# Kernel optimization log

Measured on AMD Instinct MI355X. Metric: run time of the kernel, lower is better.

The kernel has to match this reference:

```python
import jax, jax.numpy as jnp
import numpy as np
import math

B = 2        # batch
S = 4095     # input sequence (cls token makes L = 4096)
F_IN = 32    # input feature size
D = 512      # d_model (hidden_size)
H = 8        # n_heads
E = D // H   # head dim = 64
DFF = 2048   # feedforward dim
NL = 2       # encoder layers
FACTOR = 5   # probsparse sampling factor
EPS = 1e-5


def setup_inputs() -> dict:
    key = jax.random.key(0)
    ks = jax.random.split(key, 16)

    def w(k, shape):
        return jax.random.normal(k, shape, dtype=jnp.float32) * 0.02

    inp = {}
    inp['x'] = jax.random.normal(ks[0], (B, S, F_IN), dtype=jnp.float32)
    inp['We'] = w(ks[1], (D, F_IN)); inp['be'] = jnp.zeros((D,), jnp.float32)
    inp['cls'] = jnp.zeros((1, 1, D), jnp.float32)
    inp['Wq'] = w(ks[2], (NL, D, D)); inp['bq'] = jnp.zeros((NL, D), jnp.float32)
    inp['Wk'] = w(ks[3], (NL, D, D)); inp['bk'] = jnp.zeros((NL, D), jnp.float32)
    inp['Wv'] = w(ks[4], (NL, D, D)); inp['bv'] = jnp.zeros((NL, D), jnp.float32)
    inp['Wo'] = w(ks[5], (NL, D, D)); inp['bo'] = jnp.zeros((NL, D), jnp.float32)
    inp['g1'] = jnp.ones((NL, D), jnp.float32); inp['b1'] = jnp.zeros((NL, D), jnp.float32)
    inp['g2'] = jnp.ones((NL, D), jnp.float32); inp['b2'] = jnp.zeros((NL, D), jnp.float32)
    inp['W1'] = w(ks[6], (NL, DFF, D)); inp['bf1'] = jnp.zeros((NL, DFF), jnp.float32)
    inp['W2'] = w(ks[7], (NL, D, DFF)); inp['bf2'] = jnp.zeros((NL, D), jnp.float32)
    inp['Wf'] = w(ks[8], (1, D)); inp['bf'] = jnp.zeros((1,), jnp.float32)
    return inp


def pos_encoding(L):
    # Sinusoidal positional encoding [L, D]
    pos = jnp.arange(L, dtype=jnp.float32)[:, None]
    div = jnp.exp(jnp.arange(0, D, 2, dtype=jnp.float32) * (-math.log(10000.0) / D))
    pe = jnp.zeros((L, D), jnp.float32)
    pe = pe.at[:, 0::2].set(jnp.sin(pos * div))
    pe = pe.at[:, 1::2].set(jnp.cos(pos * div))
    return pe


def layer_norm(x, g, b):
    mu = x.mean(-1, keepdims=True)
    var = ((x - mu) ** 2).mean(-1, keepdims=True)
    return (x - mu) / jnp.sqrt(var + EPS) * g + b


def prob_attention(q, k, v, rng):
    # q, k, v: [B, H, L, E]; mask_flag=False (encoder self-attention)
    b, h, L, e = q.shape
    u = min(FACTOR * int(np.ceil(np.log(L))), L)  # sample_k == n_top here (L_Q == L_K)
    idx = jax.random.randint(rng, (L, u), 0, L)   # random K sampling per query position
    Ks = k[:, :, idx, :]                          # [B,H,L,u,E] gather
    QKs = jnp.einsum('bhle,bhlue->bhlu', q, Ks)   # sampled scores
    M = QKs.max(-1) - QKs.sum(-1) / L             # sparsity measure [B,H,L]
    _, top = jax.lax.top_k(M, u)                  # active query indices [B,H,u]
    Qr = jnp.take_along_axis(q, top[..., None], axis=2)      # [B,H,u,E]
    scores = jnp.einsum('bhue,bhke->bhuk', Qr, k) / math.sqrt(e)
    attn = jax.nn.softmax(scores, axis=-1)
    ctx = jnp.broadcast_to(v.mean(axis=2, keepdims=True), (b, h, L, e))  # initial context = mean(V)
    upd = jnp.einsum('bhuk,bhke->bhue', attn, v)
    bi = jnp.arange(b)[:, None, None]
    hi = jnp.arange(h)[None, :, None]
    ctx = ctx.at[bi, hi, top].set(upd)            # scatter active-query contexts
    return ctx                                    # [B,H,L,E]


def attention_layer(x, Wq_, bq_, Wk_, bk_, Wv_, bv_, Wo_, bo_, rng):
    b, L, _ = x.shape
    q = (x @ Wq_.T + bq_).reshape(b, L, H, E).transpose(0, 2, 1, 3)
    k = (x @ Wk_.T + bk_).reshape(b, L, H, E).transpose(0, 2, 1, 3)
    v = (x @ Wv_.T + bv_).reshape(b, L, H, E).transpose(0, 2, 1, 3)
    ctx = prob_attention(q, k, v, rng)            # [B,H,L,E]
    out = ctx.transpose(0, 2, 1, 3).reshape(b, L, D)
    return out @ Wo_.T + bo_


def reference(x, We, be, cls, Wq, bq, Wk, bk, Wv, bv, Wo, bo, g1, b1, g2, b2, W1, bf1, W2, bf2, Wf, bf):
    h = x @ We.T + be                                            # [B,S,D]
    h = jnp.concatenate([jnp.broadcast_to(cls, (B, 1, D)), h], axis=1)  # prepend cls
    L = h.shape[1]
    h = h + pos_encoding(L)[None]
    for l in range(NL):
        rng = jax.random.fold_in(jax.random.key(42), l)
        a = attention_layer(h, Wq[l], bq[l], Wk[l], bk[l], Wv[l], bv[l], Wo[l], bo[l], rng)
        h = layer_norm(h + a, g1[l], b1[l])
        y = jax.nn.relu(h @ W1[l].T + bf1[l])
        y = y @ W2[l].T + bf2[l]
        h = layer_norm(h + y, g2[l], b2[l])
    return h[:, 0] @ Wf.T + bf  # cls-token prediction head [B,1]
```

## Files before the change

### kernel.cpp

```cpp
#include <hip/hip_runtime.h>
#include <hip/hip_bf16.h>
#include <math.h>
#include <stdint.h>

#define B 2
#define S 4095
#define LSEQ 4096
#define F_IN 32
#define D 512
#define H 8
#define E 64
#define DFF 2048
#define NL 2
#define U 45
#define EPSL 1e-5f
#define LU (LSEQ * U)
#define HALF_LU (LU / 2)
#define NS 32
#define SLICE 128
#define CASTBLK 3074

typedef __attribute__((ext_vector_type(8))) short short8;
typedef __attribute__((ext_vector_type(4))) float f32x4;

#define GLD(gp, lp)                                                            \
    __builtin_amdgcn_global_load_lds(                                          \
        (const __attribute__((address_space(1))) void*)(gp),                   \
        (__attribute__((address_space(3))) void*)(lp), 16, 0, 0)

__device__ __forceinline__ unsigned short bf16_bits(float f) {
    __hip_bfloat16 h = __float2bfloat16(f);
    return *(unsigned short*)&h;
}
__device__ __forceinline__ float bits_to_f32(unsigned short s) {
    union { uint32_t u; float f; } c;
    c.u = ((uint32_t)s) << 16;
    return c.f;
}
__device__ __forceinline__ unsigned long long mkey(float v, int index) {
    uint32_t u = __float_as_uint(v);
    uint32_t mono = (u & 0x80000000u) ? ~u : (u | 0x80000000u);
    return ((unsigned long long)mono << 32) | (uint32_t)(0xFFFFFFFFu - (uint32_t)index);
}

#define TF_BODY(k0, k1, c0, c1, o0, o1)                                        \
    do {                                                                       \
        uint32_t ks2 = (k0) ^ (k1) ^ 0x1BD11BDAu;                              \
        uint32_t x0 = (c0) + (k0), x1 = (c1) + (k1);                           \
        x0 += x1; x1 = ((x1 << 13) | (x1 >> 19)); x1 ^= x0;                    \
        x0 += x1; x1 = ((x1 << 15) | (x1 >> 17)); x1 ^= x0;                    \
        x0 += x1; x1 = ((x1 << 26) | (x1 >> 6));  x1 ^= x0;                    \
        x0 += x1; x1 = ((x1 << 6) | (x1 >> 26));  x1 ^= x0;                    \
        x0 += (k1); x1 += ks2 + 1u;                                            \
        x0 += x1; x1 = ((x1 << 17) | (x1 >> 15)); x1 ^= x0;                    \
        x0 += x1; x1 = ((x1 << 29) | (x1 >> 3));  x1 ^= x0;                    \
        x0 += x1; x1 = ((x1 << 16) | (x1 >> 16)); x1 ^= x0;                    \
        x0 += x1; x1 = ((x1 << 24) | (x1 >> 8));  x1 ^= x0;                    \
        x0 += ks2; x1 += (k0) + 2u;                                            \
        x0 += x1; x1 = ((x1 << 13) | (x1 >> 19)); x1 ^= x0;                    \
        x0 += x1; x1 = ((x1 << 15) | (x1 >> 17)); x1 ^= x0;                    \
        x0 += x1; x1 = ((x1 << 26) | (x1 >> 6));  x1 ^= x0;                    \
        x0 += x1; x1 = ((x1 << 6) | (x1 >> 26));  x1 ^= x0;                    \
        x0 += (k0); x1 += (k1) + 3u;                                           \
        x0 += x1; x1 = ((x1 << 17) | (x1 >> 15)); x1 ^= x0;                    \
        x0 += x1; x1 = ((x1 << 29) | (x1 >> 3));  x1 ^= x0;                    \
        x0 += x1; x1 = ((x1 << 16) | (x1 >> 16)); x1 ^= x0;                    \
        x0 += x1; x1 = ((x1 << 24) | (x1 >> 8));  x1 ^= x0;                    \
        x0 += (k1); x1 += ks2 + 4u;                                            \
        x0 += x1; x1 = ((x1 << 13) | (x1 >> 19)); x1 ^= x0;                    \
        x0 += x1; x1 = ((x1 << 15) | (x1 >> 17)); x1 ^= x0;                    \
        x0 += x1; x1 = ((x1 << 26) | (x1 >> 6));  x1 ^= x0;                    \
        x0 += x1; x1 = ((x1 << 6) | (x1 >> 26));  x1 ^= x0;                    \
        x0 += ks2; x1 += (k0) + 5u;                                            \
        (o0) = x0; (o1) = x1;                                                  \
    } while (0)

__device__ __forceinline__ void threefry_dev(uint32_t k0, uint32_t k1, uint32_t c0,
                                             uint32_t c1, uint32_t& o0, uint32_t& o1) {
    TF_BODY(k0, k1, c0, c1, o0, o1);
}
static void threefry_host(uint32_t k0, uint32_t k1, uint32_t c0, uint32_t c1,
                          uint32_t& o0, uint32_t& o1) {
    TF_BODY(k0, k1, c0, c1, o0, o1);
}

__global__ void prep_cast_kernel(const float* __restrict__ x, const float* __restrict__ We,
                                 __hip_bfloat16* __restrict__ xbf,
                                 __hip_bfloat16* __restrict__ webf,
                                 const float* __restrict__ Wq,
                                 const float* __restrict__ Wk,
                                 const float* __restrict__ Wv,
                                 const float* __restrict__ Wo,
                                 const float* __restrict__ W1,
                                 const float* __restrict__ W2,
                                 const float* __restrict__ bq,
                                 const float* __restrict__ bk,
                                 const float* __restrict__ bv,
                                 __hip_bfloat16* __restrict__ wpool,
                                 float* __restrict__ qkvbias) {
    const int SDD = D * D / 4;
    const int SFD = DFF * D / 4;
    const int CAST_N = 4 * SDD + 2 * SFD;
    const size_t WPL = (size_t)4 * D * D + 2 * (size_t)DFF * D;
    int bid = blockIdx.x;
    int tid = threadIdx.x;
    if (bid < 2 * CASTBLK) {
        int l = bid / CASTBLK;
        int u = (bid % CASTBLK) * 256 + tid;
        __hip_bfloat16* base = wpool + (size_t)l * WPL;
        if (u >= CAST_N) {
            int j = u - CAST_N;
            if (j < 384) {
                int seg = (j * 4) >> 9;
                int off = (j * 4) & 511;
                const float* src = (seg == 0) ? bq + l * D
                                 : (seg == 1) ? bk + l * D : bv + l * D;
                *(float4*)(qkvbias + l * 1536 + j * 4) = *(const float4*)(src + off);
            }
            return;
        }
        const float* src;
        __hip_bfloat16* dst;
        int off;
        if (u < SDD)            { src = Wq + (size_t)l * D * D;   dst = base;                       off = u; }
        else if (u < 2 * SDD)   { src = Wk + (size_t)l * D * D;   dst = base + (size_t)D * D;       off = u - SDD; }
        else if (u < 3 * SDD)   { src = Wv + (size_t)l * D * D;   dst = base + (size_t)2 * D * D;   off = u - 2 * SDD; }
        else if (u < 4 * SDD)   { src = Wo + (size_t)l * D * D;   dst = base + (size_t)3 * D * D;   off = u - 3 * SDD; }
        else if (u < 4 * SDD + SFD) { src = W1 + (size_t)l * DFF * D; dst = base + (size_t)4 * D * D; off = u - 4 * SDD; }
        else { src = W2 + (size_t)l * D * DFF; dst = base + (size_t)4 * D * D + (size_t)DFF * D; off = u - 4 * SDD - SFD; }
        float4 v = ((const float4*)src)[off];
        union { unsigned short s[4]; uint2 w; } o;
        o.s[0] = bf16_bits(v.x); o.s[1] = bf16_bits(v.y);
        o.s[2] = bf16_bits(v.z); o.s[3] = bf16_bits(v.w);
        ((uint2*)dst)[off] = o.w;
    } else {
        int u = (bid - 2 * CASTBLK) * 256 + tid;
        const int NX = B * LSEQ * F_IN / 4;
        const int NW = D * F_IN / 4;
        if (u < NX) {
            int e0 = u * 4;
            int i = e0 & 31;
            int l = (e0 >> 5) & (LSEQ - 1);
            int b = e0 >> 17;
            union { unsigned short s[4]; uint2 w; } o;
            if (l == 0) {
                o.s[0] = o.s[1] = o.s[2] = o.s[3] = 0;
            } else {
                float4 v = *(const float4*)(x + ((size_t)b * S + (l - 1)) * F_IN + i);
                o.s[0] = bf16_bits(v.x); o.s[1] = bf16_bits(v.y);
                o.s[2] = bf16_bits(v.z); o.s[3] = bf16_bits(v.w);
            }
            ((uint2*)xbf)[u] = o.w;
        } else if (u < NX + NW) {
            int w = u - NX;
            float4 v = ((const float4*)We)[w];
            union { unsigned short s[4]; uint2 w2; } o;
            o.s[0] = bf16_bits(v.x); o.s[1] = bf16_bits(v.y);
            o.s[2] = bf16_bits(v.z); o.s[3] = bf16_bits(v.w);
            ((uint2*)webf)[w] = o.w2;
        }
    }
}

__global__ __launch_bounds__(256) void gemm32(const unsigned short* __restrict__ A,
                                              const unsigned short* __restrict__ W,
                                              const float* __restrict__ bias,
                                              float* __restrict__ Cf,
                                              int M, int N, int K) {
    __shared__ unsigned short lds[2 * 128 * 32];
    unsigned short* As = lds;
    unsigned short* Bs = lds + 128 * 32;
    const int tid = threadIdx.x;
    const int m0 = blockIdx.y * 128, n0 = blockIdx.x * 128;
    const int wave = tid >> 6, lane = tid & 63;
    const int wm = (wave >> 1) * 64, wn = (wave & 1) * 64;
    const int quad = lane >> 4, m15 = lane & 15;
    const int srow = tid >> 2, scol = (tid & 3) * 8;
    f32x4 acc[4][4] = {};
    const unsigned short* Ag0 = A + (size_t)(m0 + srow) * K + scol;
    const unsigned short* Ag1 = A + (size_t)(m0 + srow + 64) * K + scol;
    const unsigned short* Wg0 = W + (size_t)(n0 + srow) * K + scol;
    const unsigned short* Wg1 = W + (size_t)(n0 + srow + 64) * K + scol;
    for (int k0 = 0; k0 < K; k0 += 32) {
        __syncthreads();
        GLD(Ag0 + k0, As + tid * 8);
        GLD(Ag1 + k0, As + 2048 + tid * 8);
        GLD(Wg0 + k0, Bs + tid * 8);
        GLD(Wg1 + k0, Bs + 2048 + tid * 8);
        __syncthreads();
        short8 af[4], bfr[4];
#pragma unroll
        for (int mi = 0; mi < 4; ++mi)
            af[mi] = *(const short8*)(As + (wm + mi * 16 + m15) * 32 + quad * 8);
#pragma unroll
        for (int ni = 0; ni < 4; ++ni)
            bfr[ni] = *(const short8*)(Bs + (wn + ni * 16 + m15) * 32 + quad * 8);
#pragma unroll
        for (int mi = 0; mi < 4; ++mi)
#pragma unroll
            for (int ni = 0; ni < 4; ++ni)
                acc[mi][ni] = __builtin_amdgcn_mfma_f32_16x16x32_bf16(
                    af[mi], bfr[ni], acc[mi][ni], 0, 0, 0);
    }
#pragma unroll
    for (int mi = 0; mi < 4; ++mi) {
        int mg = m0 + wm + mi * 16 + quad * 4;
#pragma unroll
        for (int ni = 0; ni < 4; ++ni) {
            int ng = n0 + wn + ni * 16 + m15;
            float bv = bias[ng];
#pragma unroll
            for (int r = 0; r < 4; ++r)
                Cf[(size_t)(mg + r) * N + ng] = acc[mi][ni][r] + bv;
        }
    }
}

__global__ void posenc_kernel(const float* __restrict__ emb, const float* __restrict__ cls,
                              __hip_bfloat16* __restrict__ hbf) {
    int gid = blockIdx.x * blockDim.x + threadIdx.x;
    if (gid >= B * LSEQ * D) return;
    int d = gid % D;
    int l = (gid / D) % LSEQ;
    float v = (l == 0) ? cls[d] : emb[gid];
    int i = d >> 1;
    float divv = expf((float)(2 * i) * (float)(-9.210340371976184 / 512.0));
    float ang = (float)l * divv;
    v += (d & 1) ? cosf(ang) : sinf(ang);
    hbf[gid] = __float2bfloat16(v);
}

template <int MODE>
__global__ __launch_bounds__(256) void gemm_pipe(const unsigned short* __restrict__ A,
                                                 const unsigned short* __restrict__ W,
                                                 const float* __restrict__ bias,
                                                 void* __restrict__ C0,
                                                 void* __restrict__ C1,
                                                 void* __restrict__ C2,
                                                 int M, int N, int K, int NBN) {
    __shared__ unsigned short As[2][128 * 32];
    __shared__ unsigned short Bs[2][128 * 32];
    const int tid = threadIdx.x;
    const int NBM = M >> 7;
    const int bid = blockIdx.x;
    const int xcd = bid & 7, local = bid >> 3;
    const int m_t = xcd * (NBM >> 3) + local / NBN;
    const int n_t = local % NBN;
    const int m0 = m_t * 128, n0 = n_t * 128;
    const int wave = tid >> 6, lane = tid & 63;
    const int wm = (wave >> 1) * 64, wn = (wave & 1) * 64;
    const int quad = lane >> 4, m15 = lane & 15;
    const int srow = tid >> 2, scol = (tid & 3) * 8;
    f32x4 acc[4][4] = {};
    const unsigned short* Ag0 = A + (size_t)(m0 + srow) * K + scol;
    const unsigned short* Ag1 = A + (size_t)(m0 + srow + 64) * K + scol;
    const unsigned short* Wg0 = W + (size_t)(n0 + srow) * K + scol;
    const unsigned short* Wg1 = W + (size_t)(n0 + srow + 64) * K + scol;
    GLD(Ag0, As[0] + tid * 8);
    GLD(Ag1, As[0] + 2048 + tid * 8);
    GLD(Wg0, Bs[0] + tid * 8);
    GLD(Wg1, Bs[0] + 2048 + tid * 8);
    int cur = 0;
    for (int k0 = 0; k0 < K; k0 += 32) {
        __syncthreads();
        int kn = k0 + 32;
        if (kn < K) {
            GLD(Ag0 + kn, As[cur ^ 1] + tid * 8);
            GLD(Ag1 + kn, As[cur ^ 1] + 2048 + tid * 8);
            GLD(Wg0 + kn, Bs[cur ^ 1] + tid * 8);
            GLD(Wg1 + kn, Bs[cur ^ 1] + 2048 + tid * 8);
        }
        short8 af[4], bfr[4];
#pragma unroll
        for (int mi = 0; mi < 4; ++mi)
            af[mi] = *(const short8*)(As[cur] + (wm + mi * 16 + m15) * 32 + quad * 8);
#pragma unroll
        for (int ni = 0; ni < 4; ++ni)
            bfr[ni] = *(const short8*)(Bs[cur] + (wn + ni * 16 + m15) * 32 + quad * 8);
#pragma unroll
        for (int mi = 0; mi < 4; ++mi)
#pragma unroll
            for (int ni = 0; ni < 4; ++ni)
                acc[mi][ni] = __builtin_amdgcn_mfma_f32_16x16x32_bf16(
                    af[mi], bfr[ni], acc[mi][ni], 0, 0, 0);
        cur ^= 1;
    }
#pragma unroll
    for (int mi = 0; mi < 4; ++mi) {
        int mg = m0 + wm + mi * 16 + quad * 4;
#pragma unroll
        for (int ni = 0; ni < 4; ++ni) {
            int ng = n0 + wn + ni * 16 + m15;
            float bv = bias[ng];
#pragma unroll
            for (int r = 0; r < 4; ++r) {
                float v = acc[mi][ni][r] + bv;
                if (MODE == 1) {
                    ((__hip_bfloat16*)C0)[(size_t)(mg + r) * N + ng] = __float2bfloat16(v);
                } else if (MODE == 2) {
                    ((__hip_bfloat16*)C0)[(size_t)(mg + r) * N + ng] =
                        __float2bfloat16(fmaxf(v, 0.f));
                } else {
                    int seg = ng >> 9;
                    int col = ng & 511;
                    __hip_bfloat16* dst = (seg == 0) ? (__hip_bfloat16*)C0
                                        : (seg == 1) ? (__hip_bfloat16*)C1
                                                     : (__hip_bfloat16*)C2;
                    dst[(size_t)(mg + r) * D + col] = __float2bfloat16(v);
                }
            }
        }
    }
}

__global__ __launch_bounds__(256) void gemm_w2b(const unsigned short* __restrict__ A,
                                                const unsigned short* __restrict__ W,
                                                const float* __restrict__ bias,
                                                float* __restrict__ C0,
                                                float* __restrict__ C1) {
    const int K = 2048, N = 512, KH = 1024;
    __shared__ unsigned short As[2][128 * 32];
    __shared__ unsigned short Bs[2][128 * 32];
    const int tid = threadIdx.x;
    const int bid = blockIdx.x;
    const int xcd = bid & 7, local = bid >> 3;
    const int m_t = xcd * 8 + (local >> 3);
    const int n_t = (local >> 1) & 3;
    const int ks = local & 1;
    const int m0 = m_t * 128, n0 = n_t * 128, kb = ks * KH;
    const int wave = tid >> 6, lane = tid & 63;
    const int wm = (wave >> 1) * 64, wn = (wave & 1) * 64;
    const int quad = lane >> 4, m15 = lane & 15;
    const int srow = tid >> 2, scol = (tid & 3) * 8;
    f32x4 acc[4][4] = {};
    const unsigned short* Ag0 = A + (size_t)(m0 + srow) * K + kb + scol;
    const unsigned short* Ag1 = A + (size_t)(m0 + srow + 64) * K + kb + scol;
    const unsigned short* Wg0 = W + (size_t)(n0 + srow) * K + kb + scol;
    const unsigned short* Wg1 = W + (size_t)(n0 + srow + 64) * K + kb + scol;
    GLD(Ag0, As[0] + tid * 8);
    GLD(Ag1, As[0] + 2048 + tid * 8);
    GLD(Wg0, Bs[0] + tid * 8);
    GLD(Wg1, Bs[0] + 2048 + tid * 8);
    int cur = 0;
    for (int k0 = 0; k0 < KH; k0 += 32) {
        __syncthreads();
        int kn = k0 + 32;
        if (kn < KH) {
            GLD(Ag0 + kn, As[cur ^ 1] + tid * 8);
            GLD(Ag1 + kn, As[cur ^ 1] + 2048 + tid * 8);
            GLD(Wg0 + kn, Bs[cur ^ 1] + tid * 8);
            GLD(Wg1 + kn, Bs[cur ^ 1] + 2048 + tid * 8);
        }
        short8 af[4], bfr[4];
#pragma unroll
        for (int mi = 0; mi < 4; ++mi)
            af[mi] = *(const short8*)(As[cur] + (wm + mi * 16 + m15) * 32 + quad * 8);
#pragma unroll
        for (int ni = 0; ni < 4; ++ni)
            bfr[ni] = *(const short8*)(Bs[cur] + (wn + ni * 16 + m15) * 32 + quad * 8);
#pragma unroll
        for (int mi = 0; mi < 4; ++mi)
#pragma unroll
            for (int ni = 0; ni < 4; ++ni)
                acc[mi][ni] = __builtin_amdgcn_mfma_f32_16x16x32_bf16(
                    af[mi], bfr[ni], acc[mi][ni], 0, 0, 0);
        cur ^= 1;
    }
    float* Cf = ks ? C1 : C0;
#pragma unroll
    for (int mi = 0; mi < 4; ++mi) {
        int mg = m0 + wm + mi * 16 + quad * 4;
#pragma unroll
        for (int ni = 0; ni < 4; ++ni) {
            int ng = n0 + wn + ni * 16 + m15;
            float bv = ks ? 0.f : bias[ng];
#pragma unroll
            for (int r = 0; r < 4; ++r)
                Cf[(size_t)(mg + r) * N + ng] = acc[mi][ni][r] + bv;
        }
    }
}

__global__ __launch_bounds__(256) void mscore_kernel(const __hip_bfloat16* __restrict__ qbf,
                                                     const __hip_bfloat16* __restrict__ kbf,
                                                     uint32_t k2a, uint32_t k2b,
                                                     float* __restrict__ Mv,
                                                     float* __restrict__ acorr) {
    __shared__ float Sbuf[U][8];
    __shared__ int sidx[U];
    int bid = blockIdx.x;
    int tid = threadIdx.x;
    if (bid >= B * LSEQ) {
        int vb = bid - B * LSEQ;
        float4 z = {0.f, 0.f, 0.f, 0.f};
        float4* p = (float4*)acorr;
#pragma unroll
        for (int i = 0; i < 32; ++i)
            p[(size_t)i * 32768 + vb * 256 + tid] = z;
        return;
    }
    int b = bid & 1;
    int l = bid >> 1;
    int wave = tid >> 6, lane = tid & 63;
    if (tid < U) {
        int i = l * U + tid;
        uint32_t c0 = (i < HALF_LU) ? (uint32_t)i : (uint32_t)(i - HALF_LU);
        uint32_t o0, o1;
        threefry_dev(k2a, k2b, c0, c0 + HALF_LU, o0, o1);
        sidx[tid] = (int)(((i < HALF_LU) ? o0 : o1) & 4095u);
    }
    const unsigned short* qr =
        (const unsigned short*)qbf + ((size_t)(b * LSEQ) + l) * D + lane * 8;
    union { uint4 u; unsigned short s[8]; } qv;
    qv.u = *(const uint4*)qr;
    float qa[8];
#pragma unroll
    for (int j = 0; j < 8; ++j) qa[j] = bits_to_f32(qv.s[j]);
    __syncthreads();
    const unsigned short* kbase = (const unsigned short*)(kbf + (size_t)(b * LSEQ) * D);
    for (int t = wave; t < U; t += 12) {
        int tb = t + 4, tc = t + 8;
        bool hb = tb < U, hc = tc < U;
        union { uint4 u; unsigned short s[8]; } kva, kvb, kvc;
        kva.u = *(const uint4*)(kbase + (size_t)sidx[t] * D + lane * 8);
        if (hb) kvb.u = *(const uint4*)(kbase + (size_t)sidx[tb] * D + lane * 8);
        if (hc) kvc.u = *(const uint4*)(kbase + (size_t)sidx[tc] * D + lane * 8);
        {
            float p = 0.f;
#pragma unroll
            for (int j = 0; j < 8; ++j) p += qa[j] * bits_to_f32(kva.s[j]);
            p += __shfl_xor(p, 1);
            p += __shfl_xor(p, 2);
            p += __shfl_xor(p, 4);
            if ((lane & 7) == 0) Sbuf[t][lane >> 3] = p;
        }
        if (hb) {
            float p = 0.f;
#pragma unroll
            for (int j = 0; j < 8; ++j) p += qa[j] * bits_to_f32(kvb.s[j]);
            p += __shfl_xor(p, 1);
            p += __shfl_xor(p, 2);
            p += __shfl_xor(p, 4);
            if ((lane & 7) == 0) Sbuf[tb][lane >> 3] = p;
        }
        if (hc) {
            float p = 0.f;
#pragma unroll
            for (int j = 0; j < 8; ++j) p += qa[j] * bits_to_f32(kvc.s[j]);
            p += __shfl_xor(p, 1);
            p += __shfl_xor(p, 2);
            p += __shfl_xor(p, 4);
            if ((lane & 7) == 0) Sbuf[tc][lane >> 3] = p;
        }
    }
    __syncthreads();
    if (tid < 8) {
        float mx = -INFINITY, sm = 0.f;
        for (int t = 0; t < U; ++t) {
            float v = Sbuf[t][tid];
            mx = fmaxf(mx, v);
            sm += v;
        }
        Mv[((size_t)b * H + tid) * LSEQ + l] = mx - sm / (float)LSEQ;
    }
}

__global__ __launch_bounds__(256) void topk_chunk_kernel(const float* __restrict__ Mv,
                                                         unsigned long long* __restrict__ cand) {
    __shared__ unsigned long long sk[256];
    int blk = blockIdx.x;
    int chunk = blk & 15, bh = blk >> 4;
    int tid = threadIdx.x;
    int gi = chunk * 256 + tid;
    sk[tid] = mkey(Mv[(size_t)bh * LSEQ + gi], gi);
    __syncthreads();
    for (int k = 2; k <= 256; k <<= 1) {
        for (int j = k >> 1; j > 0; j >>= 1) {
            int ixj = tid ^ j;
            if (ixj > tid) {
                unsigned long long a = sk[tid], b = sk[ixj];
                bool desc = ((tid & k) == 0);
                if (desc ? (a < b) : (a > b)) { sk[tid] = b; sk[ixj] = a; }
            }
            __syncthreads();
        }
    }
    if (tid < U) cand[((size_t)bh * 16 + chunk) * U + tid] = sk[tid];
}

__global__ __launch_bounds__(256) void topkmerge_vmean_kernel(
        const unsigned long long* __restrict__ cand, int* __restrict__ top,
        const __hip_bfloat16* __restrict__ v, float* __restrict__ part,
        unsigned char* __restrict__ flags) {
    __shared__ unsigned long long sk[1024];
    __shared__ float red[4][64];
    int blk = blockIdx.x;
    int tid = threadIdx.x;
    if (blk < B * H) {
        int bh = blk;
        for (int e = tid; e < 1024; e += 256)
            sk[e] = (e < 16 * U) ? cand[(size_t)bh * 16 * U + e] : 0ull;
        __syncthreads();
        for (int k = 2; k <= 1024; k <<= 1) {
            for (int j = k >> 1; j > 0; j >>= 1) {
                for (int e = tid; e < 1024; e += 256) {
                    int ixj = e ^ j;
                    if (ixj > e) {
                        unsigned long long a = sk[e], b = sk[ixj];
                        bool desc = ((e & k) == 0);
                        if (desc ? (a < b) : (a > b)) { sk[e] = b; sk[ixj] = a; }
                    }
                }
                __syncthreads();
            }
        }
        if (tid < U)
            top[bh * U + tid] = (int)(0xFFFFFFFFu - (uint32_t)(sk[tid] & 0xFFFFFFFFu));
    } else if (blk < B * H + B * H * 8) {
        int vb = blk - B * H;
        int seg = vb & 7, hh = (vb >> 3) & 7, b = vb >> 6;
        int e = tid & 63, rg = tid >> 6;
        const __hip_bfloat16* vp =
            v + ((size_t)(b * LSEQ) + seg * 512) * D + hh * 64 + e;
        float acc = 0.f;
        for (int r = rg; r < 512; r += 4) acc += __bfloat162float(vp[(size_t)r * D]);
        red[rg][e] = acc;
        __syncthreads();
        if (tid < 64)
            part[(size_t)vb * 64 + tid] =
                red[0][tid] + red[1][tid] + red[2][tid] + red[3][tid];
    } else {
        int fb = blk - (B * H + B * H * 8);
        ((int*)flags)[fb * 256 + tid] = 0;
    }
}

__global__ __launch_bounds__(256) void attnred_wobase_kernel(
        const float* __restrict__ Opart, const float* __restrict__ msum,
        const float* __restrict__ vpart, const unsigned short* __restrict__ wob,
        const int* __restrict__ top, float* __restrict__ acorr,
        unsigned char* __restrict__ flags, const float* __restrict__ bo,
        float* __restrict__ base) {
    __shared__ float dlt[E];
    int bid = blockIdx.x;
    int tid = threadIdx.x;
    if (bid < B * H * U) {
        int t = bid % U;
        int bh = bid / U;
        int b = bh >> 3, hh = bh & 7;
        if (tid < 64) {
            int lane = tid;
            float m_s = -INFINITY, ss = 0.f;
            if (lane < NS) {
                size_t base2 = (((size_t)bh * NS + lane) * U + t) * 2;
                m_s = msum[base2];
                ss = msum[base2 + 1];
            }
            float M = m_s;
            for (int off = 32; off; off >>= 1) M = fmaxf(M, __shfl_xor(M, off));
            float e_s = (lane < NS) ? __expf(m_s - M) : 0.f;
            float d = ss * e_s;
            for (int off = 32; off; off >>= 1) d += __shfl_xor(d, off);
            float acc = 0.f;
            for (int s = 0; s < NS; ++s) {
                float w = __shfl(e_s, s);
                acc += w * Opart[(((size_t)bh * NS + s) * U + t) * 64 + lane];
            }
            float vmv = 0.f;
#pragma unroll
            for (int s = 0; s < 8; ++s) vmv += vpart[((size_t)bh * 8 + s) * 64 + lane];
            dlt[lane] = acc / d - vmv / (float)LSEQ;
        }
        __syncthreads();
        int r = top[bh * U + t];
        if (tid == 0) flags[b * LSEQ + r] = 1;
        float* arow = acorr + (size_t)(b * LSEQ + r) * D;
        for (int n = tid; n < D; n += 256) {
            const unsigned short* wr = wob + (size_t)n * D + hh * E;
            float acc = 0.f;
#pragma unroll
            for (int v4 = 0; v4 < 8; ++v4) {
                union { uint4 u; unsigned short s[8]; } w;
                w.u = *(const uint4*)(wr + v4 * 8);
#pragma unroll
                for (int j = 0; j < 8; ++j)
                    acc += dlt[v4 * 8 + j] * bits_to_f32(w.s[j]);
            }
            atomicAdd(arow + n, acc);
        }
    } else {
        int wb = bid - B * H * U;
        int b = wb >> 7;
        int n = (wb & 127) * 4 + (tid >> 6);
        int lane = tid & 63;
        float vmv[8];
#pragma unroll
        for (int j = 0; j < 8; ++j) {
            int idx = lane * 8 + j;
            int hh = idx >> 6, e = idx & 63;
            float acc = 0.f;
#pragma unroll
            for (int s = 0; s < 8; ++s)
                acc += vpart[((size_t)(b * 8 + hh) * 8 + s) * 64 + e];
            vmv[j] = acc / (float)LSEQ;
        }
        union { uint4 u; unsigned short s[8]; } w;
        w.u = *(const uint4*)(wob + (size_t)n * D + lane * 8);
        float p = vmv[0] * bits_to_f32(w.s[0]) + vmv[1] * bits_to_f32(w.s[1]) +
                  vmv[2] * bits_to_f32(w.s[2]) + vmv[3] * bits_to_f32(w.s[3]) +
                  vmv[4] * bits_to_f32(w.s[4]) + vmv[5] * bits_to_f32(w.s[5]) +
                  vmv[6] * bits_to_f32(w.s[6]) + vmv[7] * bits_to_f32(w.s[7]);
        for (int off = 32; off; off >>= 1) p += __shfl_xor(p, off);
        if (lane == 0) base[(size_t)b * D + n] = p + bo[n];
    }
}

__global__ __launch_bounds__(256) void attn_part(const __hip_bfloat16* __restrict__ qbf,
                                                 const __hip_bfloat16* __restrict__ kbf,
                                                 const __hip_bfloat16* __restrict__ vbf,
                                                 const int* __restrict__ top,
                                                 float* __restrict__ Opart,
                                                 float* __restrict__ msum) {
    __shared__ unsigned short Qs[48 * 72];
    __shared__ unsigned short Ks[SLICE * 72];
    __shared__ unsigned short Vs[SLICE * 68];
    __shared__ unsigned short Ps[48 * 136];
    __shared__ float mred[48][4];
    __shared__ float sred[48][4];
    const int slice = blockIdx.x, hh = blockIdx.y, b = blockIdx.z;
    const int bh = b * H + hh;
    const int tid = threadIdx.x;
    const int s0 = slice * SLICE;
    for (int i = tid; i < 48 * 64; i += 256) {
        int t = i >> 6, e = i & 63;
        unsigned short v = 0;
        if (t < U) {
            int r = top[bh * U + t];
            v = ((const unsigned short*)qbf)[((size_t)(b * LSEQ) + r) * D + hh * E + e];
        }
        Qs[t * 72 + e] = v;
    }
    {
        const uint4* src = (const uint4*)(kbf + ((size_t)(b * LSEQ) + s0) * D + hh * E);
        for (int i = tid; i < SLICE * 8; i += 256) {
            int r = i >> 3, c = i & 7;
            uint4 d = src[(size_t)r * 64 + c];
            *(uint4*)(Ks + r * 72 + c * 8) = d;
        }
    }
    {
        const uint2* src = (const uint2*)(vbf + ((size_t)(b * LSEQ) + s0) * D + hh * E);
        for (int i = tid; i < SLICE * 16; i += 256) {
            int r = i >> 4, c = i & 15;
            uint2 d = src[(size_t)r * 128 + c];
            *(uint2*)(Vs + r * 68 + c * 4) = d;
        }
    }
    __syncthreads();
    const int wave = tid >> 6, lane = tid & 63;
    const int quad = lane >> 4, m15 = lane & 15;
    const int wc = wave * 32;
    f32x4 acc[3][2] = {};
#pragma unroll
    for (int ks = 0; ks < 2; ++ks) {
        short8 af[3], bfr[2];
#pragma unroll
        for (int mt = 0; mt < 3; ++mt)
            af[mt] = *(const short8*)(Qs + (mt * 16 + m15) * 72 + ks * 32 + quad * 8);
#pragma unroll
        for (int nt = 0; nt < 2; ++nt)
            bfr[nt] = *(const short8*)(Ks + (wc + nt * 16 + m15) * 72 + ks * 32 + quad * 8);
#pragma unroll
        for (int mt = 0; mt < 3; ++mt)
#pragma unroll
            for (int nt = 0; nt < 2; ++nt)
                acc[mt][nt] = __builtin_amdgcn_mfma_f32_16x16x32_bf16(
                    af[mt], bfr[nt], acc[mt][nt], 0, 0, 0);
    }
    float sc[3][2][4];
#pragma unroll
    for (int mt = 0; mt < 3; ++mt)
#pragma unroll
        for (int nt = 0; nt < 2; ++nt)
#pragma unroll
            for (int r = 0; r < 4; ++r) sc[mt][nt][r] = acc[mt][nt][r] * 0.125f;
#pragma unroll
    for (int mt = 0; mt < 3; ++mt)
#pragma unroll
        for (int r = 0; r < 4; ++r) {
            float mv = fmaxf(sc[mt][0][r], sc[mt][1][r]);
            mv = fmaxf(mv, __shfl_xor(mv, 1));
            mv = fmaxf(mv, __shfl_xor(mv, 2));
            mv = fmaxf(mv, __shfl_xor(mv, 4));
            mv = fmaxf(mv, __shfl_xor(mv, 8));
            if (m15 == 0) mred[mt * 16 + quad * 4 + r][wave] = mv;
        }
    __syncthreads();
#pragma unroll
    for (int mt = 0; mt < 3; ++mt)
#pragma unroll
        for (int r = 0; r < 4; ++r) {
            int row = mt * 16 + quad * 4 + r;
            float ms = fmaxf(fmaxf(mred[row][0], mred[row][1]),
                             fmaxf(mred[row][2], mred[row][3]));
            float p0 = __expf(sc[mt][0][r] - ms);
            float p1 = __expf(sc[mt][1][r] - ms);
            float sv = p0 + p1;
            sv += __shfl_xor(sv, 1);
            sv += __shfl_xor(sv, 2);
            sv += __shfl_xor(sv, 4);
            sv += __shfl_xor(sv, 8);
            if (m15 == 0) sred[row][wave] = sv;
            Ps[row * 136 + wc + m15] = bf16_bits(p0);
            Ps[row * 136 + wc + 16 + m15] = bf16_bits(p1);
        }
    __syncthreads();
    if (tid < U) {
        float mm = fmaxf(fmaxf(mred[tid][0], mred[tid][1]),
                         fmaxf(mred[tid][2], mred[tid][3]));
        float ss = sred[tid][0] + sred[tid][1] + sred[tid][2] + sred[tid][3];
        size_t base = (((size_t)bh * NS + slice) * U + tid) * 2;
        msum[base] = mm;
        msum[base + 1] = ss;
    }
    f32x4 apv[3] = {};
#pragma unroll
    for (int ks = 0; ks < 4; ++ks) {
        short8 bv;
#pragma unroll
        for (int j = 0; j < 8; ++j)
            bv[j] = (short)Vs[(ks * 32 + quad * 8 + j) * 68 + wave * 16 + m15];
        short8 af2[3];
#pragma unroll
        for (int mt = 0; mt < 3; ++mt)
            af2[mt] = *(const short8*)(Ps + (mt * 16 + m15) * 136 + ks * 32 + quad * 8);
#pragma unroll
        for (int mt = 0; mt < 3; ++mt)
            apv[mt] = __builtin_amdgcn_mfma_f32_16x16x32_bf16(af2[mt], bv, apv[mt], 0, 0, 0);
    }
    size_t obase = ((size_t)bh * NS + slice) * U;
#pragma unroll
    for (int mt = 0; mt < 3; ++mt)
#pragma unroll
        for (int r = 0; r < 4; ++r) {
            int row = mt * 16 + quad * 4 + r;
            if (row < U)
                Opart[(obase + row) * 64 + wave * 16 + m15] = apv[mt][r];
        }
}

__global__ __launch_bounds__(64) void add_ln_base_kernel(__hip_bfloat16* __restrict__ hbf,
                                                         const float* __restrict__ base,
                                                         const float* __restrict__ acorr,
                                                         const unsigned char* __restrict__ flags,
                                                         const float* __restrict__ g,
                                                         const float* __restrict__ bb) {
    int row = blockIdx.x;
    int b = row >> 12;
    int lane = threadIdx.x;
    unsigned short* hp = (unsigned short*)hbf + (size_t)row * D;
    const float* bp = base + (size_t)b * D;
    const float* ap = acorr + (size_t)row * D;
    bool has = flags[row] != 0;
    float x[8];
    float sum = 0.f;
#pragma unroll
    for (int j = 0; j < 8; ++j) {
        float a = bp[lane + 64 * j];
        if (has) a += ap[lane + 64 * j];
        x[j] = bits_to_f32(hp[lane + 64 * j]) + a;
        sum += x[j];
    }
    for (int off = 32; off; off >>= 1) sum += __shfl_xor(sum, off);
    float mu = sum / (float)D;
    float vs = 0.f;
#pragma unroll
    for (int j = 0; j < 8; ++j) {
        float dd = x[j] - mu;
        vs += dd * dd;
    }
    for (int off = 32; off; off >>= 1) vs += __shfl_xor(vs, off);
    float inv = 1.f / sqrtf(vs / (float)D + EPSL);
#pragma unroll
    for (int j = 0; j < 8; ++j) {
        float o = (x[j] - mu) * inv * g[lane + 64 * j] + bb[lane + 64 * j];
        hp[lane + 64 * j] = bf16_bits(o);
    }
}

__global__ __launch_bounds__(64) void add_ln_kernel(__hip_bfloat16* __restrict__ hbf,
                                                    const float* __restrict__ a,
                                                    const float* __restrict__ a2,
                                                    const float* __restrict__ g,
                                                    const float* __restrict__ bb,
                                                    const float* __restrict__ Wf,
                                                    const float* __restrict__ bf,
                                                    float* __restrict__ out,
                                                    int fuseFinal) {
    int row = blockIdx.x;
    int lane = threadIdx.x;
    unsigned short* hp = (unsigned short*)hbf + (size_t)row * D;
    const float* ap = a + (size_t)row * D;
    const float* ap2 = a2 + (size_t)row * D;
    float x[8];
    float sum = 0.f;
#pragma unroll
    for (int j = 0; j < 8; ++j) {
        x[j] = bits_to_f32(hp[lane + 64 * j]) + ap[lane + 64 * j] + ap2[lane + 64 * j];
        sum += x[j];
    }
    for (int off = 32; off; off >>= 1) sum += __shfl_xor(sum, off);
    float mu = sum / (float)D;
    float vs = 0.f;
#pragma unroll
    for (int j = 0; j < 8; ++j) {
        float dd = x[j] - mu;
        vs += dd * dd;
    }
    for (int off = 32; off; off >>= 1) vs += __shfl_xor(vs, off);
    float inv = 1.f / sqrtf(vs / (float)D + EPSL);
    bool doFinal = fuseFinal && ((row & (LSEQ - 1)) == 0);
    float facc = 0.f;
#pragma unroll
    for (int j = 0; j < 8; ++j) {
        float o = (x[j] - mu) * inv * g[lane + 64 * j] + bb[lane + 64 * j];
        unsigned short ob = bf16_bits(o);
        hp[lane + 64 * j] = ob;
        if (doFinal) facc += bits_to_f32(ob) * Wf[lane + 64 * j];
    }
    if (doFinal) {
        for (int off = 32; off; off >>= 1) facc += __shfl_xor(facc, off);
        if (lane == 0) out[row >> 12] = facc + bf[0];
    }
}

extern "C" void kernel_launch(void* const* d_in, const int* in_sizes, int n_in,
                              void* d_out, int out_size, void* d_ws, size_t ws_size,
                              hipStream_t stream) {
    (void)in_sizes; (void)n_in; (void)out_size; (void)ws_size;
    const float* x   = (const float*)d_in[0];
    const float* We  = (const float*)d_in[1];
    const float* be  = (const float*)d_in[2];
    const float* cls = (const float*)d_in[3];
    const float* Wq  = (const float*)d_in[4];
    const float* bq  = (const float*)d_in[5];
    const float* Wk  = (const float*)d_in[6];
    const float* bk  = (const float*)d_in[7];
    const float* Wv  = (const float*)d_in[8];
    const float* bv  = (const float*)d_in[9];
    const float* Wo  = (const float*)d_in[10];
    const float* bo  = (const float*)d_in[11];
    const float* g1  = (const float*)d_in[12];
    const float* b1  = (const float*)d_in[13];
    const float* g2  = (const float*)d_in[14];
    const float* b2  = (const float*)d_in[15];
    const float* W1  = (const float*)d_in[16];
    const float* bf1 = (const float*)d_in[17];
    const float* W2  = (const float*)d_in[18];
    const float* bf2 = (const float*)d_in[19];
    const float* Wf  = (const float*)d_in[20];
    const float* bff = (const float*)d_in[21];
    float* out = (float*)d_out;

    float* ws = (float*)d_ws;
    const size_t NT = (size_t)B * LSEQ * D;
    float* aout = ws + NT;
    __hip_bfloat16* kbf    = (__hip_bfloat16*)(ws + NT);
    __hip_bfloat16* q_bf   = (__hip_bfloat16*)(ws + 2 * NT);
    __hip_bfloat16* y1_bf  = (__hip_bfloat16*)(ws + 2 * NT);
    __hip_bfloat16* v_bf   = (__hip_bfloat16*)(ws + 4 * NT);
    __hip_bfloat16* h_bf   = (__hip_bfloat16*)(ws + 5 * NT);
    float* emb   = ws;
    float* acorr = ws;
    float* tmp   = ws;
    float* Opart = ws + 3 * NT;
    float* msumb = Opart + (size_t)B * H * NS * U * 64;
    float* wpool = ws + 5 * NT + NT / 2;
    const size_t WPL = (size_t)4 * D * D + 2 * (size_t)DFF * D;
    __hip_bfloat16* wpool_bf = (__hip_bfloat16*)wpool;
    float* after_w = wpool + (2 * WPL) / 2;
    float* Mbuf = after_w;
    int* top    = (int*)(Mbuf + (size_t)B * H * LSEQ);
    float* vpart  = (float*)(top + B * H * U);
    float* baseb  = vpart + (size_t)128 * 64;
    __hip_bfloat16* xbf  = (__hip_bfloat16*)(baseb + (size_t)B * D);
    __hip_bfloat16* webf = xbf + (size_t)B * LSEQ * F_IN;
    unsigned long long* cand =
        (unsigned long long*)(((uintptr_t)(webf + (size_t)D * F_IN) + 7) & ~(uintptr_t)7);
    float* qkvbias = (float*)(cand + (size_t)B * H * 16 * U);
    unsigned char* flags = (unsigned char*)(qkvbias + 2 * 1536);

    const int ML = B * LSEQ;
    dim3 gD(D / 128, ML / 128);
    const int NPREP = (B * LSEQ * F_IN / 4 + D * F_IN / 4 + 255) / 256;

    prep_cast_kernel<<<2 * CASTBLK + NPREP, 256, 0, stream>>>(
        x, We, xbf, webf, Wq, Wk, Wv, Wo, W1, W2, bq, bk, bv, wpool_bf, qkvbias);
    gemm32<<<gD, 256, 0, stream>>>((const unsigned short*)xbf,
                                   (const unsigned short*)webf, be, emb, ML, D, F_IN);
    posenc_kernel<<<(B * LSEQ * D + 255) / 256, 256, 0, stream>>>(emb, cls, h_bf);

    for (int l = 0; l < NL; ++l) {
        uint32_t f0, f1, a0, a1, bb0, bb1;
        threefry_host(0u, 42u, 0u, (uint32_t)l, f0, f1);
        threefry_host(f0, f1, 0u, 2u, a0, a1);
        threefry_host(f0, f1, 1u, 3u, bb0, bb1);
        (void)a0; (void)bb0;

        __hip_bfloat16* wqb = wpool_bf + (size_t)l * WPL;
        __hip_bfloat16* wob = wqb + (size_t)3 * D * D;
        __hip_bfloat16* w1b = wqb + (size_t)4 * D * D;
        __hip_bfloat16* w2b = w1b + (size_t)DFF * D;

        gemm_pipe<3><<<768, 256, 0, stream>>>((const unsigned short*)h_bf,
                                              (const unsigned short*)wqb,
                                              qkvbias + (size_t)l * 1536,
                                              q_bf, kbf, v_bf, ML, 3 * D, D, 12);

        mscore_kernel<<<B * LSEQ + 128, 256, 0, stream>>>(q_bf, kbf, a1, bb1, Mbuf,
                                                          acorr);
        topk_chunk_kernel<<<B * H * 16, 256, 0, stream>>>(Mbuf, cand);
        topkmerge_vmean_kernel<<<B * H + B * H * 8 + 8, 256, 0, stream>>>(
            cand, top, v_bf, vpart, flags);
        attn_part<<<dim3(NS, H, B), 256, 0, stream>>>(q_bf, kbf, v_bf, top, Opart, msumb);
        attnred_wobase_kernel<<<B * H * U + B * 128, 256, 0, stream>>>(
            Opart, msumb, vpart, (const unsigned short*)wob, top, acorr, flags,
            bo + l * D, baseb);
        add_ln_base_kernel<<<ML, 64, 0, stream>>>(h_bf, baseb, acorr, flags,
                                                  g1 + l * D, b1 + l * D);

        gemm_pipe<2><<<1024, 256, 0, stream>>>((const unsigned short*)h_bf,
                                               (const unsigned short*)w1b, bf1 + l * DFF,
                                               y1_bf, nullptr, nullptr, ML, DFF, D, 16);
        gemm_w2b<<<512, 256, 0, stream>>>((const unsigned short*)y1_bf,
                                          (const unsigned short*)w2b, bf2 + l * D,
                                          aout, tmp);
        add_ln_kernel<<<ML, 64, 0, stream>>>(h_bf, aout, tmp, g2 + l * D, b2 + l * D,
                                             Wf, bff, out, (l == NL - 1) ? 1 : 0);
    }
}
```

Before: 541.8 us.

## Triple-buffer GEMM shared-memory loads with explicit vmcnt waits

Changes the bf16 MFMA GEMM from double to triple buffering in LDS. Global-to-LDS loads for two tiles ahead are issued, and explicit s_waitcnt vmcnt counts wait only for the current tile, so more memory latency is hidden behind compute. A second barrier after the fragment reads lets the next prefetch overwrite buffers safely. LDS use grows by half, which may reduce occupancy, and the extra barrier per iteration adds sync cost.

```diff
diff --git a/kernel.cpp b/kernel.cpp
--- a/kernel.cpp
+++ b/kernel.cpp
@@ -238,8 +238,8 @@
                                                  void* __restrict__ C1,
                                                  void* __restrict__ C2,
                                                  int M, int N, int K, int NBN) {
-    __shared__ unsigned short As[2][128 * 32];
-    __shared__ unsigned short Bs[2][128 * 32];
+    __shared__ unsigned short As[3][128 * 32];
+    __shared__ unsigned short Bs[3][128 * 32];
     const int tid = threadIdx.x;
     const int NBM = M >> 7;
     const int bid = blockIdx.x;
@@ -256,20 +256,26 @@
     const unsigned short* Ag1 = A + (size_t)(m0 + srow + 64) * K + scol;
     const unsigned short* Wg0 = W + (size_t)(n0 + srow) * K + scol;
     const unsigned short* Wg1 = W + (size_t)(n0 + srow + 64) * K + scol;
-    GLD(Ag0, As[0] + tid * 8);
-    GLD(Ag1, As[0] + 2048 + tid * 8);
-    GLD(Wg0, Bs[0] + tid * 8);
-    GLD(Wg1, Bs[0] + 2048 + tid * 8);
-    int cur = 0;
-    for (int k0 = 0; k0 < K; k0 += 32) {
-        __syncthreads();
-        int kn = k0 + 32;
-        if (kn < K) {
-            GLD(Ag0 + kn, As[cur ^ 1] + tid * 8);
-            GLD(Ag1 + kn, As[cur ^ 1] + 2048 + tid * 8);
-            GLD(Wg0 + kn, Bs[cur ^ 1] + tid * 8);
-            GLD(Wg1 + kn, Bs[cur ^ 1] + 2048 + tid * 8);
-        }
+#define STAGE_P(buf, k0)                                                       \
+    do {                                                                       \
+        GLD(Ag0 + (k0), As[buf] + tid * 8);                                    \
+        GLD(Ag1 + (k0), As[buf] + 2048 + tid * 8);                             \
+        GLD(Wg0 + (k0), Bs[buf] + tid * 8);                                    \
+        GLD(Wg1 + (k0), Bs[buf] + 2048 + tid * 8);                             \
+    } while (0)
+    const int NIT = K >> 5;
+    STAGE_P(0, 0);
+    STAGE_P(1, 32);
+    for (int i = 0; i < NIT; ++i) {
+        int cur = i % 3;
+        if (i + 2 < NIT) STAGE_P((i + 2) % 3, (i + 2) * 32);
+        int rem = NIT - 1 - i;
+        if (rem >= 2)      asm volatile("s_waitcnt vmcnt(8)" ::: "memory");
+        else if (rem == 1) asm volatile("s_waitcnt vmcnt(4)" ::: "memory");
+        else               asm volatile("s_waitcnt vmcnt(0)" ::: "memory");
+        __builtin_amdgcn_sched_barrier(0);
+        __builtin_amdgcn_s_barrier();
+        __builtin_amdgcn_sched_barrier(0);
         short8 af[4], bfr[4];
 #pragma unroll
         for (int mi = 0; mi < 4; ++mi)
@@ -277,14 +283,18 @@
 #pragma unroll
         for (int ni = 0; ni < 4; ++ni)
             bfr[ni] = *(const short8*)(Bs[cur] + (wn + ni * 16 + m15) * 32 + quad * 8);
+        asm volatile("s_waitcnt lgkmcnt(0)" ::: "memory");
+        __builtin_amdgcn_sched_barrier(0);
+        __builtin_amdgcn_s_barrier();
+        __builtin_amdgcn_sched_barrier(0);
 #pragma unroll
         for (int mi = 0; mi < 4; ++mi)
 #pragma unroll
             for (int ni = 0; ni < 4; ++ni)
                 acc[mi][ni] = __builtin_amdgcn_mfma_f32_16x16x32_bf16(
                     af[mi], bfr[ni], acc[mi][ni], 0, 0, 0);
-        cur ^= 1;
-    }
+    }
+#undef STAGE_P
 #pragma unroll
     for (int mi = 0; mi < 4; ++mi) {
         int mg = m0 + wm + mi * 16 + quad * 4;
```

After: 542.9 us, median of 2. No clear change (+0.2%).
